# Kernel optimization log

Measured on AMD Instinct MI355X. Metric: run time of the kernel, lower is better.

The kernel has to match this reference:

```python
import jax, jax.numpy as jnp
import numpy as np

N = 100000   # nodes
E = 1600000  # edges
D = 64       # feature dim (input = hidden = output)
G = 256      # graphs in batch
EPS = 1e-5   # BatchNorm eps


def setup_inputs() -> dict:
    key = jax.random.key(0)
    ks = jax.random.split(key, 16)
    inp = {
        "x": jax.random.normal(ks[0], (N, D), dtype=jnp.float32),
        "edge_index": jax.random.randint(ks[1], (2, E), 0, N, dtype=jnp.int64),
        "batch": jnp.sort(jax.random.randint(ks[2], (N,), 0, G, dtype=jnp.int64)),
    }
    # GCNConv weights (glorot-ish) + biases, and BatchNorm affine params, 3 layers
    for i in range(3):
        inp[f"W{i+1}"] = jax.random.normal(ks[3 + i], (D, D), dtype=jnp.float32) / np.sqrt(D)
        inp[f"b{i+1}"] = jnp.zeros((D,), dtype=jnp.float32)
        inp[f"g{i+1}"] = jnp.ones((D,), dtype=jnp.float32)   # BN gamma
        inp[f"be{i+1}"] = jnp.zeros((D,), dtype=jnp.float32)  # BN beta
    return inp


def _batchnorm(x, gamma, beta):
    # BatchNorm1d in training mode: batch stats over the node dim (biased var)
    mean = jnp.mean(x, axis=0)
    var = jnp.mean(jnp.square(x - mean), axis=0)
    return (x - mean) * jax.lax.rsqrt(var + EPS) * gamma + beta


def reference(x, edge_index, batch, W1, b1, g1, be1, W2, b2, g2, be2, W3, b3, g3, be3):
    src, dst = edge_index[0], edge_index[1]
    # GCN normalization with self-loops: norm_ij = deg_i^-1/2 * deg_j^-1/2 over A + I
    loop = jnp.arange(N, dtype=src.dtype)
    src2 = jnp.concatenate([src, loop])
    dst2 = jnp.concatenate([dst, loop])
    deg = jax.ops.segment_sum(jnp.ones_like(src2, dtype=x.dtype), dst2, num_segments=N)
    dinv = jax.lax.rsqrt(deg)  # deg >= 1 thanks to self loops
    norm = (dinv[src2] * dinv[dst2])[:, None]  # [E+N, 1]

    def gcn_conv(h, W, b):
        h = h @ W                                   # [N, D] small GEMM
        msg = h[src2] * norm                        # per-edge gather (memory bound)
        return jax.ops.segment_sum(msg, dst2, num_segments=N) + b

    params = [(W1, b1, g1, be1), (W2, b2, g2, be2), (W3, b3, g3, be3)]
    h = x
    for i, (W, b, g, be) in enumerate(params):
        h = gcn_conv(h, W, b)
        h = _batchnorm(h, g, be)
        if i < 2:
            h = jax.nn.relu(h)
            # dropout(p=0.2) is identity in deterministic/eval reference

    # global mean + max pool per graph
    ones = jnp.ones((N,), dtype=h.dtype)
    cnt = jax.ops.segment_sum(ones, batch, num_segments=G)            # [G]
    s = jax.ops.segment_sum(h, batch, num_segments=G)                 # [G, D]
    mean = s / jnp.maximum(cnt, 1.0)[:, None]
    mx = jax.ops.segment_max(h, batch, num_segments=G)
    mx = jnp.where(cnt[:, None] > 0, mx, 0.0)
    return mean + mx
```

## Files before the change

kernel.cpp:

```cpp
#include <hip/hip_runtime.h>
#include <hip/hip_bf16.h>
#include <math.h>

#define N_NODES 100000
#define N_EDGES 1600000
#define DIM 64
#define N_GRAPHS 256
#define BN_EPS 1e-5f
#define N_XCD 8
#define BUCKET ((N_NODES + N_XCD - 1) / N_XCD)
#define FILL_CHUNKS 128
#define FILL_ESIZE ((N_EDGES + FILL_CHUNKS - 1) / FILL_CHUNKS)
#define CSR_STRIDE 48
#define HIST_BLOCKS (FILL_CHUNKS * N_XCD)
#define GEMM0_BLOCKS 1024

__device__ inline unsigned short f2bf(float f) {
    __hip_bfloat16 h = __float2bfloat16(f);
    return *reinterpret_cast<unsigned short*>(&h);
}
__device__ inline unsigned int pack2bf(float a, float b) {
    return (unsigned int)f2bf(a) | ((unsigned int)f2bf(b) << 16);
}
__device__ inline float bf_lo(unsigned int u) { return __uint_as_float(u << 16); }
__device__ inline float bf_hi(unsigned int u) { return __uint_as_float(u & 0xffff0000u); }

__global__ __launch_bounds__(256) void hist_gemm0(const int* __restrict__ src,
                                                  const int* __restrict__ dst,
                                                  int* __restrict__ cnt,
                                                  int* __restrict__ csr_pad,
                                                  const float* __restrict__ x,
                                                  const float* __restrict__ W,
                                                  unsigned short* __restrict__ tb) {
    if (blockIdx.x < HIST_BLOCKS) {
        int chunk = blockIdx.x >> 3;
        int lo = (blockIdx.x & (N_XCD - 1)) * BUCKET;
        int e0 = chunk * FILL_ESIZE;
        int e1 = min(e0 + FILL_ESIZE, N_EDGES);
        for (int e = e0 + threadIdx.x; e < e1; e += 256) {
            int d = __builtin_nontemporal_load(&dst[e]);
            if ((unsigned)(d - lo) < (unsigned)BUCKET) {
                int r = atomicAdd(&cnt[d], 1);
                csr_pad[d * CSR_STRIDE + r] = __builtin_nontemporal_load(&src[e]);
            }
        }
    } else {
        int tid = threadIdx.x;
        int d = tid & 63;
        int wv = tid >> 6;
        float wcol[64];
        #pragma unroll
        for (int k = 0; k < 64; ++k) wcol[k] = W[k * 64 + d];
        int gb = blockIdx.x - HIST_BLOCKS;
        int nwaves = GEMM0_BLOCKS * 4;
        for (int row = gb * 4 + wv; row < N_NODES; row += nwaves) {
            int urow = __builtin_amdgcn_readfirstlane(row);
            const float* hr = x + (size_t)urow * 64;
            float a0 = 0.f, a1 = 0.f, a2 = 0.f, a3 = 0.f;
            #pragma unroll
            for (int k = 0; k < 64; k += 4) {
                a0 = fmaf(hr[k + 0], wcol[k + 0], a0);
                a1 = fmaf(hr[k + 1], wcol[k + 1], a1);
                a2 = fmaf(hr[k + 2], wcol[k + 2], a2);
                a3 = fmaf(hr[k + 3], wcol[k + 3], a3);
            }
            float acc = (a0 + a1) + (a2 + a3);
            tb[(size_t)urow * 64 + d] = f2bf(acc);
        }
    }
}

__global__ __launch_bounds__(256) void finish_scale(const int* __restrict__ cnt,
                                                    unsigned short* __restrict__ tb,
                                                    float* __restrict__ dinv) {
    const int total = N_NODES * 8;
    for (int i = blockIdx.x * 256 + threadIdx.x; i < total; i += gridDim.x * 256) {
        int row = i >> 3;
        float di = rsqrtf((float)(cnt[row] + 1));
        uint4 u = *reinterpret_cast<const uint4*>(tb + (size_t)i * 8);
        uint4 o;
        o.x = pack2bf(bf_lo(u.x) * di, bf_hi(u.x) * di);
        o.y = pack2bf(bf_lo(u.y) * di, bf_hi(u.y) * di);
        o.z = pack2bf(bf_lo(u.z) * di, bf_hi(u.z) * di);
        o.w = pack2bf(bf_lo(u.w) * di, bf_hi(u.w) * di);
        *reinterpret_cast<uint4*>(tb + (size_t)i * 8) = o;
        if ((i & 7) == 0) dinv[row] = di;
    }
}

__global__ __launch_bounds__(256) void bn_gemm_v(const unsigned short* __restrict__ hb,
                                                 const float* __restrict__ stats,
                                                 const float* __restrict__ gamma,
                                                 const float* __restrict__ beta,
                                                 const float* __restrict__ W,
                                                 const float* __restrict__ dinv,
                                                 unsigned short* __restrict__ tb) {
    __shared__ float abuf[4][64];
    __shared__ float scale_s[64], shift_s[64];
    int tid = threadIdx.x;
    int d = tid & 63;
    int wv = tid >> 6;
    if (tid < 64) {
        const float inv_n = 1.0f / (float)N_NODES;
        float mean = stats[tid] * inv_n;
        float var = fmaxf(stats[64 + tid] * inv_n - mean * mean, 0.f);
        float rs = rsqrtf(var + BN_EPS) * gamma[tid];
        scale_s[tid] = rs;
        shift_s[tid] = beta[tid] - mean * rs;
    }
    float wcol[64];
    #pragma unroll
    for (int k = 0; k < 64; ++k) wcol[k] = W[k * 64 + d];
    __syncthreads();
    float sc = scale_s[d], sh = shift_s[d];
    const float4* av = reinterpret_cast<const float4*>(abuf[wv]);
    int nwaves = gridDim.x * 4;
    int row = blockIdx.x * 4 + wv;
    unsigned short hraw = 0;
    if (row < N_NODES) hraw = hb[(size_t)row * 64 + d];
    while (row < N_NODES) {
        int nrow = row + nwaves;
        unsigned short hnraw = 0;
        if (nrow < N_NODES) hnraw = hb[(size_t)nrow * 64 + d];
        float di = dinv[row];
        float h = __uint_as_float(((unsigned int)hraw) << 16);
        float a = fmaxf(fmaf(h, sc, sh), 0.f);
        abuf[wv][d] = a;
        float a0 = 0.f, a1 = 0.f, a2 = 0.f, a3 = 0.f;
        #pragma unroll
        for (int k4 = 0; k4 < 16; ++k4) {
            float4 v = av[k4];
            int k = k4 * 4;
            a0 = fmaf(v.x, wcol[k + 0], a0);
            a1 = fmaf(v.y, wcol[k + 1], a1);
            a2 = fmaf(v.z, wcol[k + 2], a2);
            a3 = fmaf(v.w, wcol[k + 3], a3);
        }
        float acc = (a0 + a1) + (a2 + a3);
        tb[(size_t)row * 64 + d] = f2bf(acc * di);
        row = nrow;
        hraw = hnraw;
    }
}

__global__ __launch_bounds__(256) void gather_agg(const int* __restrict__ csr_pad,
                                                  const int* __restrict__ cnt,
                                                  const float* __restrict__ dinv,
                                                  const unsigned short* __restrict__ tb,
                                                  const float* __restrict__ bias,
                                                  unsigned short* __restrict__ out,
                                                  float* __restrict__ stats) {
    int tid = threadIdx.x;
    int wave = tid >> 6;
    int lane = tid & 63;
    int q    = lane >> 4;
    int ql   = lane & 15;

    float4 s4  = {0.f, 0.f, 0.f, 0.f};
    float4 sq4 = {0.f, 0.f, 0.f, 0.f};

    for (int v = blockIdx.x * 4 + wave; v < N_NODES; v += gridDim.x * 4) {
        int beg = v * CSR_STRIDE;
        int end = beg + cnt[v];
        float4 acc  = {0.f, 0.f, 0.f, 0.f};
        float4 acc2 = {0.f, 0.f, 0.f, 0.f};
        int e = beg + q;
        for (; e + 4 < end; e += 8) {
            int s0 = csr_pad[e];
            int s1 = csr_pad[e + 4];
            uint2 u0 = *reinterpret_cast<const uint2*>(tb + (size_t)s0 * 64 + ql * 4);
            uint2 u1 = *reinterpret_cast<const uint2*>(tb + (size_t)s1 * 64 + ql * 4);
            acc.x  += bf_lo(u0.x); acc.y  += bf_hi(u0.x);
            acc.z  += bf_lo(u0.y); acc.w  += bf_hi(u0.y);
            acc2.x += bf_lo(u1.x); acc2.y += bf_hi(u1.x);
            acc2.z += bf_lo(u1.y); acc2.w += bf_hi(u1.y);
        }
        if (e < end) {
            int s0 = csr_pad[e];
            uint2 u0 = *reinterpret_cast<const uint2*>(tb + (size_t)s0 * 64 + ql * 4);
            acc.x += bf_lo(u0.x); acc.y += bf_hi(u0.x);
            acc.z += bf_lo(u0.y); acc.w += bf_hi(u0.y);
        }
        acc.x += acc2.x; acc.y += acc2.y; acc.z += acc2.z; acc.w += acc2.w;

        acc.x += __shfl_xor(acc.x, 16, 64); acc.x += __shfl_xor(acc.x, 32, 64);
        acc.y += __shfl_xor(acc.y, 16, 64); acc.y += __shfl_xor(acc.y, 32, 64);
        acc.z += __shfl_xor(acc.z, 16, 64); acc.z += __shfl_xor(acc.z, 32, 64);
        acc.w += __shfl_xor(acc.w, 16, 64); acc.w += __shfl_xor(acc.w, 32, 64);

        if (q == 0) {
            float di = dinv[v];
            uint2 uv = *reinterpret_cast<const uint2*>(tb + (size_t)v * 64 + ql * 4);
            float4 bi = *reinterpret_cast<const float4*>(bias + ql * 4);
            float4 val;
            val.x = fmaf(di, acc.x + bf_lo(uv.x), bi.x);
            val.y = fmaf(di, acc.y + bf_hi(uv.x), bi.y);
            val.z = fmaf(di, acc.z + bf_lo(uv.y), bi.z);
            val.w = fmaf(di, acc.w + bf_hi(uv.y), bi.w);
            uint2 o;
            o.x = pack2bf(val.x, val.y);
            o.y = pack2bf(val.z, val.w);
            *reinterpret_cast<uint2*>(out + (size_t)v * 64 + ql * 4) = o;
            s4.x += val.x; s4.y += val.y; s4.z += val.z; s4.w += val.w;
            sq4.x += val.x * val.x; sq4.y += val.y * val.y;
            sq4.z += val.z * val.z; sq4.w += val.w * val.w;
        }
    }

    __shared__ float shs[4][64];
    __shared__ float shq[4][64];
    if (q == 0) {
        *reinterpret_cast<float4*>(&shs[wave][ql * 4]) = s4;
        *reinterpret_cast<float4*>(&shq[wave][ql * 4]) = sq4;
    }
    __syncthreads();
    if (tid < 64) {
        float S = shs[0][tid] + shs[1][tid] + shs[2][tid] + shs[3][tid];
        float Q = shq[0][tid] + shq[1][tid] + shq[2][tid] + shq[3][tid];
        unsafeAtomicAdd(&stats[tid], S);
        unsafeAtomicAdd(&stats[64 + tid], Q);
    }
}

__global__ __launch_bounds__(256) void pool_partial(const unsigned short* __restrict__ hb,
                                                    const int* __restrict__ batch,
                                                    const float* __restrict__ stats,
                                                    const float* __restrict__ gamma,
                                                    const float* __restrict__ beta,
                                                    float* __restrict__ pS,
                                                    float* __restrict__ pM) {
    int bid = blockIdx.x;
    int g = bid >> 2, p = bid & 3;
    __shared__ float scale[64], shift[64];
    __shared__ int bounds[2];
    int tid = threadIdx.x;
    if (tid < 64) {
        const float inv_n = 1.0f / (float)N_NODES;
        float mean = stats[tid] * inv_n;
        float var = fmaxf(stats[64 + tid] * inv_n - mean * mean, 0.f);
        float rs = rsqrtf(var + BN_EPS) * gamma[tid];
        scale[tid] = rs;
        shift[tid] = beta[tid] - mean * rs;
    }
    if (tid < 2) {
        int target = g + tid;
        int lo = 0, hi = N_NODES;
        while (lo < hi) {
            int mid = (lo + hi) >> 1;
            if (batch[mid] < target) lo = mid + 1; else hi = mid;
        }
        bounds[tid] = lo;
    }
    __syncthreads();
    int lo = bounds[0], hi = bounds[1];
    int d = tid & 63, g4 = tid >> 6;
    float sc = scale[d], sh = shift[d];
    float s = 0.f, m = -3.402823466e38f;
    for (int row = lo + p * 4 + g4; row < hi; row += 16) {
        float v = __uint_as_float(((unsigned int)hb[(size_t)row * 64 + d]) << 16);
        v = fmaf(v, sc, sh);
        s += v;
        m = fmaxf(m, v);
    }
    __shared__ float shs[8][64];
    shs[g4][d] = s;
    shs[4 + g4][d] = m;
    __syncthreads();
    if (tid < 64) {
        float S = shs[0][tid] + shs[1][tid] + shs[2][tid] + shs[3][tid];
        float M = fmaxf(fmaxf(shs[4][tid], shs[5][tid]), fmaxf(shs[6][tid], shs[7][tid]));
        pS[bid * 64 + tid] = S;
        pM[bid * 64 + tid] = M;
    }
}

__global__ __launch_bounds__(64) void pool_final(const int* __restrict__ batch,
                                                 const float* __restrict__ pS,
                                                 const float* __restrict__ pM,
                                                 float* __restrict__ out) {
    int g = blockIdx.x, d = threadIdx.x;
    __shared__ int bounds[2];
    if (d < 2) {
        int target = g + d;
        int lo = 0, hi = N_NODES;
        while (lo < hi) {
            int mid = (lo + hi) >> 1;
            if (batch[mid] < target) lo = mid + 1; else hi = mid;
        }
        bounds[d] = lo;
    }
    __syncthreads();
    int cnt = bounds[1] - bounds[0];
    int base = g * 4 * 64 + d;
    float S = (pS[base] + pS[base + 64]) + (pS[base + 128] + pS[base + 192]);
    float M = fmaxf(fmaxf(pM[base], pM[base + 64]), fmaxf(pM[base + 128], pM[base + 192]));
    float mean = S / fmaxf((float)cnt, 1.0f);
    out[g * 64 + d] = (cnt > 0) ? (mean + M) : 0.0f;
}

extern "C" void kernel_launch(void* const* d_in, const int* in_sizes, int n_in,
                              void* d_out, int out_size, void* d_ws, size_t ws_size,
                              hipStream_t stream) {
    const float* x     = (const float*)d_in[0];
    const int*   eidx  = (const int*)d_in[1];
    const int*   batch = (const int*)d_in[2];
    const float* W[3]  = {(const float*)d_in[3], (const float*)d_in[7],  (const float*)d_in[11]};
    const float* b[3]  = {(const float*)d_in[4], (const float*)d_in[8],  (const float*)d_in[12]};
    const float* gm[3] = {(const float*)d_in[5], (const float*)d_in[9],  (const float*)d_in[13]};
    const float* be[3] = {(const float*)d_in[6], (const float*)d_in[10], (const float*)d_in[14]};

    unsigned short* tb    = (unsigned short*)d_ws;
    unsigned short* agg   = tb + (size_t)N_NODES * 64;
    float* dinv     = (float*)(agg + (size_t)N_NODES * 64);
    float* stats    = dinv + N_NODES;
    int*   cnt      = (int*)(stats + 384);
    float* poolS    = (float*)(cnt + N_NODES);
    float* poolM    = poolS + 1024 * 64;
    int*   csr_pad  = (int*)(poolM + 1024 * 64);

    const int* srcp = eidx;
    const int* dstp = eidx + N_EDGES;

    hipMemsetAsync(stats, 0, (384 + N_NODES) * sizeof(float), stream);

    hist_gemm0<<<HIST_BLOCKS + GEMM0_BLOCKS, 256, 0, stream>>>(srcp, dstp, cnt, csr_pad,
                                                               x, W[0], tb);
    finish_scale<<<1024, 256, 0, stream>>>(cnt, tb, dinv);

    gather_agg<<<2048, 256, 0, stream>>>(csr_pad, cnt, dinv, tb, b[0], agg, stats);

    bn_gemm_v<<<1024, 256, 0, stream>>>(agg, stats, gm[0], be[0], W[1], dinv, tb);
    gather_agg<<<2048, 256, 0, stream>>>(csr_pad, cnt, dinv, tb, b[1], agg, stats + 128);

    bn_gemm_v<<<1024, 256, 0, stream>>>(agg, stats + 128, gm[1], be[1], W[2], dinv, tb);
    gather_agg<<<2048, 256, 0, stream>>>(csr_pad, cnt, dinv, tb, b[2], agg, stats + 256);

    pool_partial<<<N_GRAPHS * 4, 256, 0, stream>>>(agg, batch, stats + 256, gm[2], be[2], poolS, poolM);
    pool_final<<<N_GRAPHS, 64, 0, stream>>>(batch, poolS, poolM, (float*)d_out);
}
```

Baseline: 443.6 us.

## Split feature tables into two 32-column halves for cache-local gathers

Stores the bf16 transformed features and aggregated outputs as two separate half-width arrays (columns 0-31 and 32-63). Each gather block now processes only one half, with blocks interleaved so that half the blocks in each group of 8 take each half. Every gathered row shrinks to 64 bytes and each half table is 6.4MB, so the randomly accessed working set is more likely to stay resident in L2 or the XCD-local cache. The cost is that every CSR index is read twice and there are more wave iterations and shuffle steps per node.

New measurement: 425.7 us (median of 2 runs). 4.0% less time.

```diff
diff --git a/kernel.cpp b/kernel.cpp
--- a/kernel.cpp
+++ b/kernel.cpp
@@ -31,7 +31,8 @@
                                                   int* __restrict__ csr_pad,
                                                   const float* __restrict__ x,
                                                   const float* __restrict__ W,
-                                                  unsigned short* __restrict__ tb) {
+                                                  unsigned short* __restrict__ tbA,
+                                                  unsigned short* __restrict__ tbB) {
     if (blockIdx.x < HIST_BLOCKS) {
         int chunk = blockIdx.x >> 3;
         int lo = (blockIdx.x & (N_XCD - 1)) * BUCKET;
@@ -51,6 +52,7 @@
         float wcol[64];
         #pragma unroll
         for (int k = 0; k < 64; ++k) wcol[k] = W[k * 64 + d];
+        unsigned short* tdst = (d < 32) ? (tbA + d) : (tbB + (d - 32));
         int gb = blockIdx.x - HIST_BLOCKS;
         int nwaves = GEMM0_BLOCKS * 4;
         for (int row = gb * 4 + wv; row < N_NODES; row += nwaves) {
@@ -65,36 +67,42 @@
                 a3 = fmaf(hr[k + 3], wcol[k + 3], a3);
             }
             float acc = (a0 + a1) + (a2 + a3);
-            tb[(size_t)urow * 64 + d] = f2bf(acc);
+            tdst[(size_t)urow * 32] = f2bf(acc);
         }
     }
 }
 
 __global__ __launch_bounds__(256) void finish_scale(const int* __restrict__ cnt,
-                                                    unsigned short* __restrict__ tb,
+                                                    unsigned short* __restrict__ tbA,
+                                                    unsigned short* __restrict__ tbB,
                                                     float* __restrict__ dinv) {
-    const int total = N_NODES * 8;
-    for (int i = blockIdx.x * 256 + threadIdx.x; i < total; i += gridDim.x * 256) {
-        int row = i >> 3;
+    const int per_arr = N_NODES * 4;
+    for (int i = blockIdx.x * 256 + threadIdx.x; i < 2 * per_arr; i += gridDim.x * 256) {
+        int second = (i >= per_arr);
+        int j = second ? (i - per_arr) : i;
+        int row = j >> 2;
         float di = rsqrtf((float)(cnt[row] + 1));
-        uint4 u = *reinterpret_cast<const uint4*>(tb + (size_t)i * 8);
+        unsigned short* p = (second ? tbB : tbA) + (size_t)j * 8;
+        uint4 u = *reinterpret_cast<const uint4*>(p);
         uint4 o;
         o.x = pack2bf(bf_lo(u.x) * di, bf_hi(u.x) * di);
         o.y = pack2bf(bf_lo(u.y) * di, bf_hi(u.y) * di);
         o.z = pack2bf(bf_lo(u.z) * di, bf_hi(u.z) * di);
         o.w = pack2bf(bf_lo(u.w) * di, bf_hi(u.w) * di);
-        *reinterpret_cast<uint4*>(tb + (size_t)i * 8) = o;
-        if ((i & 7) == 0) dinv[row] = di;
-    }
-}
-
-__global__ __launch_bounds__(256) void bn_gemm_v(const unsigned short* __restrict__ hb,
+        *reinterpret_cast<uint4*>(p) = o;
+        if (!second && (j & 3) == 0) dinv[row] = di;
+    }
+}
+
+__global__ __launch_bounds__(256) void bn_gemm_v(const unsigned short* __restrict__ aggA,
+                                                 const unsigned short* __restrict__ aggB,
                                                  const float* __restrict__ stats,
                                                  const float* __restrict__ gamma,
                                                  const float* __restrict__ beta,
                                                  const float* __restrict__ W,
                                                  const float* __restrict__ dinv,
-                                                 unsigned short* __restrict__ tb) {
+                                                 unsigned short* __restrict__ tbA,
+                                                 unsigned short* __restrict__ tbB) {
     __shared__ float abuf[4][64];
     __shared__ float scale_s[64], shift_s[64];
     int tid = threadIdx.x;
@@ -113,15 +121,17 @@
     for (int k = 0; k < 64; ++k) wcol[k] = W[k * 64 + d];
     __syncthreads();
     float sc = scale_s[d], sh = shift_s[d];
+    const unsigned short* hsrc = (d < 32) ? (aggA + d) : (aggB + (d - 32));
+    unsigned short* tdst = (d < 32) ? (tbA + d) : (tbB + (d - 32));
     const float4* av = reinterpret_cast<const float4*>(abuf[wv]);
     int nwaves = gridDim.x * 4;
     int row = blockIdx.x * 4 + wv;
     unsigned short hraw = 0;
-    if (row < N_NODES) hraw = hb[(size_t)row * 64 + d];
+    if (row < N_NODES) hraw = hsrc[(size_t)row * 32];
     while (row < N_NODES) {
         int nrow = row + nwaves;
         unsigned short hnraw = 0;
-        if (nrow < N_NODES) hnraw = hb[(size_t)nrow * 64 + d];
+        if (nrow < N_NODES) hnraw = hsrc[(size_t)nrow * 32];
         float di = dinv[row];
         float h = __uint_as_float(((unsigned int)hraw) << 16);
         float a = fmaxf(fmaf(h, sc, sh), 0.f);
@@ -137,7 +147,7 @@
             a3 = fmaf(v.w, wcol[k + 3], a3);
         }
         float acc = (a0 + a1) + (a2 + a3);
-        tb[(size_t)row * 64 + d] = f2bf(acc * di);
+        tdst[(size_t)row * 32] = f2bf(acc * di);
         row = nrow;
         hraw = hnraw;
     }
@@ -146,83 +156,89 @@
 __global__ __launch_bounds__(256) void gather_agg(const int* __restrict__ csr_pad,
                                                   const int* __restrict__ cnt,
                                                   const float* __restrict__ dinv,
-                                                  const unsigned short* __restrict__ tb,
+                                                  const unsigned short* __restrict__ tbA,
+                                                  const unsigned short* __restrict__ tbB,
                                                   const float* __restrict__ bias,
-                                                  unsigned short* __restrict__ out,
+                                                  unsigned short* __restrict__ aggA,
+                                                  unsigned short* __restrict__ aggB,
                                                   float* __restrict__ stats) {
     int tid = threadIdx.x;
     int wave = tid >> 6;
     int lane = tid & 63;
-    int q    = lane >> 4;
-    int ql   = lane & 15;
+    int o    = lane >> 3;
+    int c    = lane & 7;
+
+    int g8   = blockIdx.x & 7;
+    int half = (g8 >= 4) ? 1 : 0;
+    int hbid = (blockIdx.x >> 3) * 4 + (g8 & 3);
+    const unsigned short* tbH  = half ? tbB : tbA;
+    unsigned short*       aggH = half ? aggB : aggA;
+    const float*          biH  = bias + half * 32;
 
     float4 s4  = {0.f, 0.f, 0.f, 0.f};
     float4 sq4 = {0.f, 0.f, 0.f, 0.f};
 
-    for (int v = blockIdx.x * 4 + wave; v < N_NODES; v += gridDim.x * 4) {
+    for (int v = hbid * 4 + wave; v < N_NODES; v += 4096) {
         int beg = v * CSR_STRIDE;
         int end = beg + cnt[v];
-        float4 acc  = {0.f, 0.f, 0.f, 0.f};
-        float4 acc2 = {0.f, 0.f, 0.f, 0.f};
-        int e = beg + q;
-        for (; e + 4 < end; e += 8) {
-            int s0 = csr_pad[e];
-            int s1 = csr_pad[e + 4];
-            uint2 u0 = *reinterpret_cast<const uint2*>(tb + (size_t)s0 * 64 + ql * 4);
-            uint2 u1 = *reinterpret_cast<const uint2*>(tb + (size_t)s1 * 64 + ql * 4);
-            acc.x  += bf_lo(u0.x); acc.y  += bf_hi(u0.x);
-            acc.z  += bf_lo(u0.y); acc.w  += bf_hi(u0.y);
-            acc2.x += bf_lo(u1.x); acc2.y += bf_hi(u1.x);
-            acc2.z += bf_lo(u1.y); acc2.w += bf_hi(u1.y);
-        }
-        if (e < end) {
-            int s0 = csr_pad[e];
-            uint2 u0 = *reinterpret_cast<const uint2*>(tb + (size_t)s0 * 64 + ql * 4);
-            acc.x += bf_lo(u0.x); acc.y += bf_hi(u0.x);
-            acc.z += bf_lo(u0.y); acc.w += bf_hi(u0.y);
-        }
-        acc.x += acc2.x; acc.y += acc2.y; acc.z += acc2.z; acc.w += acc2.w;
-
-        acc.x += __shfl_xor(acc.x, 16, 64); acc.x += __shfl_xor(acc.x, 32, 64);
-        acc.y += __shfl_xor(acc.y, 16, 64); acc.y += __shfl_xor(acc.y, 32, 64);
-        acc.z += __shfl_xor(acc.z, 16, 64); acc.z += __shfl_xor(acc.z, 32, 64);
-        acc.w += __shfl_xor(acc.w, 16, 64); acc.w += __shfl_xor(acc.w, 32, 64);
-
-        if (q == 0) {
+        float4 A = {0,0,0,0}, B = {0,0,0,0};
+        int e = beg;
+        for (; e + 16 <= end; e += 16) {
+            int s0 = csr_pad[e + o];
+            int s1 = csr_pad[e + 8 + o];
+            uint2 u0 = *reinterpret_cast<const uint2*>(tbH + (size_t)s0 * 32 + c * 4);
+            uint2 u1 = *reinterpret_cast<const uint2*>(tbH + (size_t)s1 * 32 + c * 4);
+            A.x += bf_lo(u0.x); A.y += bf_hi(u0.x); A.z += bf_lo(u0.y); A.w += bf_hi(u0.y);
+            B.x += bf_lo(u1.x); B.y += bf_hi(u1.x); B.z += bf_lo(u1.y); B.w += bf_hi(u1.y);
+        }
+        for (; e + o < end; e += 8) {
+            int s0 = csr_pad[e + o];
+            uint2 u0 = *reinterpret_cast<const uint2*>(tbH + (size_t)s0 * 32 + c * 4);
+            A.x += bf_lo(u0.x); A.y += bf_hi(u0.x); A.z += bf_lo(u0.y); A.w += bf_hi(u0.y);
+        }
+        A.x += B.x; A.y += B.y; A.z += B.z; A.w += B.w;
+
+        A.x += __shfl_xor(A.x, 8, 64); A.x += __shfl_xor(A.x, 16, 64); A.x += __shfl_xor(A.x, 32, 64);
+        A.y += __shfl_xor(A.y, 8, 64); A.y += __shfl_xor(A.y, 16, 64); A.y += __shfl_xor(A.y, 32, 64);
+        A.z += __shfl_xor(A.z, 8, 64); A.z += __shfl_xor(A.z, 16, 64); A.z += __shfl_xor(A.z, 32, 64);
+        A.w += __shfl_xor(A.w, 8, 64); A.w += __shfl_xor(A.w, 16, 64); A.w += __shfl_xor(A.w, 32, 64);
+
+        if (o == 0) {
             float di = dinv[v];
-            uint2 uv = *reinterpret_cast<const uint2*>(tb + (size_t)v * 64 + ql * 4);
-            float4 bi = *reinterpret_cast<const float4*>(bias + ql * 4);
+            uint2 uv = *reinterpret_cast<const uint2*>(tbH + (size_t)v * 32 + c * 4);
+            float4 bi = *reinterpret_cast<const float4*>(biH + c * 4);
             float4 val;
-            val.x = fmaf(di, acc.x + bf_lo(uv.x), bi.x);
-            val.y = fmaf(di, acc.y + bf_hi(uv.x), bi.y);
-            val.z = fmaf(di, acc.z + bf_lo(uv.y), bi.z);
-            val.w = fmaf(di, acc.w + bf_hi(uv.y), bi.w);
-            uint2 o;
-            o.x = pack2bf(val.x, val.y);
-            o.y = pack2bf(val.z, val.w);
-            *reinterpret_cast<uint2*>(out + (size_t)v * 64 + ql * 4) = o;
+            val.x = fmaf(di, A.x + bf_lo(uv.x), bi.x);
+            val.y = fmaf(di, A.y + bf_hi(uv.x), bi.y);
+            val.z = fmaf(di, A.z + bf_lo(uv.y), bi.z);
+            val.w = fmaf(di, A.w + bf_hi(uv.y), bi.w);
+            uint2 ov;
+            ov.x = pack2bf(val.x, val.y);
+            ov.y = pack2bf(val.z, val.w);
+            *reinterpret_cast<uint2*>(aggH + (size_t)v * 32 + c * 4) = ov;
             s4.x += val.x; s4.y += val.y; s4.z += val.z; s4.w += val.w;
             sq4.x += val.x * val.x; sq4.y += val.y * val.y;
             sq4.z += val.z * val.z; sq4.w += val.w * val.w;
         }
     }
 
-    __shared__ float shs[4][64];
-    __shared__ float shq[4][64];
-    if (q == 0) {
-        *reinterpret_cast<float4*>(&shs[wave][ql * 4]) = s4;
-        *reinterpret_cast<float4*>(&shq[wave][ql * 4]) = sq4;
-    }
-    __syncthreads();
-    if (tid < 64) {
+    __shared__ float shs[4][32];
+    __shared__ float shq[4][32];
+    if (o == 0) {
+        *reinterpret_cast<float4*>(&shs[wave][c * 4]) = s4;
+        *reinterpret_cast<float4*>(&shq[wave][c * 4]) = sq4;
+    }
+    __syncthreads();
+    if (tid < 32) {
         float S = shs[0][tid] + shs[1][tid] + shs[2][tid] + shs[3][tid];
         float Q = shq[0][tid] + shq[1][tid] + shq[2][tid] + shq[3][tid];
-        unsafeAtomicAdd(&stats[tid], S);
-        unsafeAtomicAdd(&stats[64 + tid], Q);
-    }
-}
-
-__global__ __launch_bounds__(256) void pool_partial(const unsigned short* __restrict__ hb,
+        unsafeAtomicAdd(&stats[half * 32 + tid], S);
+        unsafeAtomicAdd(&stats[64 + half * 32 + tid], Q);
+    }
+}
+
+__global__ __launch_bounds__(256) void pool_partial(const unsigned short* __restrict__ aggA,
+                                                    const unsigned short* __restrict__ aggB,
                                                     const int* __restrict__ batch,
                                                     const float* __restrict__ stats,
                                                     const float* __restrict__ gamma,
@@ -254,10 +270,11 @@
     __syncthreads();
     int lo = bounds[0], hi = bounds[1];
     int d = tid & 63, g4 = tid >> 6;
+    const unsigned short* hsrc = (d < 32) ? (aggA + d) : (aggB + (d - 32));
     float sc = scale[d], sh = shift[d];
     float s = 0.f, m = -3.402823466e38f;
     for (int row = lo + p * 4 + g4; row < hi; row += 16) {
-        float v = __uint_as_float(((unsigned int)hb[(size_t)row * 64 + d]) << 16);
+        float v = __uint_as_float(((unsigned int)hsrc[(size_t)row * 32]) << 16);
         v = fmaf(v, sc, sh);
         s += v;
         m = fmaxf(m, v);
@@ -309,9 +326,11 @@
     const float* gm[3] = {(const float*)d_in[5], (const float*)d_in[9],  (const float*)d_in[13]};
     const float* be[3] = {(const float*)d_in[6], (const float*)d_in[10], (const float*)d_in[14]};
 
-    unsigned short* tb    = (unsigned short*)d_ws;
-    unsigned short* agg   = tb + (size_t)N_NODES * 64;
-    float* dinv     = (float*)(agg + (size_t)N_NODES * 64);
+    unsigned short* tbA   = (unsigned short*)d_ws;
+    unsigned short* tbB   = tbA + (size_t)N_NODES * 32;
+    unsigned short* aggA  = tbB + (size_t)N_NODES * 32;
+    unsigned short* aggB  = aggA + (size_t)N_NODES * 32;
+    float* dinv     = (float*)(aggB + (size_t)N_NODES * 32);
     float* stats    = dinv + N_NODES;
     int*   cnt      = (int*)(stats + 384);
     float* poolS    = (float*)(cnt + N_NODES);
@@ -324,17 +343,17 @@
     hipMemsetAsync(stats, 0, (384 + N_NODES) * sizeof(float), stream);
 
     hist_gemm0<<<HIST_BLOCKS + GEMM0_BLOCKS, 256, 0, stream>>>(srcp, dstp, cnt, csr_pad,
-                                                               x, W[0], tb);
-    finish_scale<<<1024, 256, 0, stream>>>(cnt, tb, dinv);
-
-    gather_agg<<<2048, 256, 0, stream>>>(csr_pad, cnt, dinv, tb, b[0], agg, stats);
-
-    bn_gemm_v<<<1024, 256, 0, stream>>>(agg, stats, gm[0], be[0], W[1], dinv, tb);
-    gather_agg<<<2048, 256, 0, stream>>>(csr_pad, cnt, dinv, tb, b[1], agg, stats + 128);
-
-    bn_gemm_v<<<1024, 256, 0, stream>>>(agg, stats + 128, gm[1], be[1], W[2], dinv, tb);
-    gather_agg<<<2048, 256, 0, stream>>>(csr_pad, cnt, dinv, tb, b[2], agg, stats + 256);
-
-    pool_partial<<<N_GRAPHS * 4, 256, 0, stream>>>(agg, batch, stats + 256, gm[2], be[2], poolS, poolM);
+                                                               x, W[0], tbA, tbB);
+    finish_scale<<<1024, 256, 0, stream>>>(cnt, tbA, tbB, dinv);
+
+    gather_agg<<<2048, 256, 0, stream>>>(csr_pad, cnt, dinv, tbA, tbB, b[0], aggA, aggB, stats);
+
+    bn_gemm_v<<<1024, 256, 0, stream>>>(aggA, aggB, stats, gm[0], be[0], W[1], dinv, tbA, tbB);
+    gather_agg<<<2048, 256, 0, stream>>>(csr_pad, cnt, dinv, tbA, tbB, b[1], aggA, aggB, stats + 128);
+
+    bn_gemm_v<<<1024, 256, 0, stream>>>(aggA, aggB, stats + 128, gm[1], be[1], W[2], dinv, tbA, tbB);
+    gather_agg<<<2048, 256, 0, stream>>>(csr_pad, cnt, dinv, tbA, tbB, b[2], aggA, aggB, stats + 256);
+
+    pool_partial<<<N_GRAPHS * 4, 256, 0, stream>>>(aggA, aggB, batch, stats + 256, gm[2], be[2], poolS, poolM);
     pool_final<<<N_GRAPHS, 64, 0, stream>>>(batch, poolS, poolM, (float*)d_out);
 }
```
